# Kernel tuning notes

Hardware: AMD Instinct MI355X
Metric: run time of the kernel (lower is better)

## Reference

```python
import jax, jax.numpy as jnp
import numpy as np

WIN_SIZE = 11
SIGMA = 1.5
WEIGHTS = np.array([0.0448, 0.2856, 0.3001, 0.2363, 0.1333], dtype=np.float32)
K1, K2 = 0.01, 0.03
DATA_RANGE = 255.0
C1 = (K1 * DATA_RANGE) ** 2
C2 = (K2 * DATA_RANGE) ** 2
N_SCALES = 5


def _gauss1d():
    coords = np.arange(WIN_SIZE, dtype=np.float32) - WIN_SIZE // 2
    g = np.exp(-(coords ** 2) / (2.0 * SIGMA ** 2))
    g /= g.sum()
    return jnp.asarray(g, dtype=jnp.float32)


def _blur(x, g):
    # separable depthwise gaussian blur, VALID padding (matches pytorch_msssim)
    C = x.shape[1]
    wh = jnp.tile(g.reshape(1, 1, 1, WIN_SIZE), (C, 1, 1, 1))
    wv = jnp.tile(g.reshape(1, 1, WIN_SIZE, 1), (C, 1, 1, 1))
    dn = ('NCHW', 'OIHW', 'NCHW')
    x = jax.lax.conv_general_dilated(x, wh, (1, 1), 'VALID', dimension_numbers=dn, feature_group_count=C)
    x = jax.lax.conv_general_dilated(x, wv, (1, 1), 'VALID', dimension_numbers=dn, feature_group_count=C)
    return x


def _ssim(X, Y, g):
    mu1 = _blur(X, g)
    mu2 = _blur(Y, g)
    mu1_sq = mu1 * mu1
    mu2_sq = mu2 * mu2
    mu1_mu2 = mu1 * mu2
    sigma1_sq = _blur(X * X, g) - mu1_sq
    sigma2_sq = _blur(Y * Y, g) - mu2_sq
    sigma12 = _blur(X * Y, g) - mu1_mu2
    cs_map = (2.0 * sigma12 + C2) / (sigma1_sq + sigma2_sq + C2)
    ssim_map = ((2.0 * mu1_mu2 + C1) / (mu1_sq + mu2_sq + C1)) * cs_map
    return ssim_map.mean(axis=(2, 3)), cs_map.mean(axis=(2, 3))  # [B,C] each


def _avg_pool2(x):
    # avg_pool2d kernel=2 stride=2; H,W chosen even at every scale so padding=0
    return jax.lax.reduce_window(x, 0.0, jax.lax.add, (1, 1, 2, 2), (1, 1, 2, 2), 'VALID') / 4.0


def setup_inputs() -> dict:
    key = jax.random.key(0)
    k1, k2 = jax.random.split(key)
    shape = (32, 3, 384, 384)
    prediction = jax.random.uniform(k1, shape, dtype=jnp.float32) * DATA_RANGE
    truth = jax.random.uniform(k2, shape, dtype=jnp.float32) * DATA_RANGE
    return {"prediction": prediction, "truth": truth}


def reference(prediction, truth):
    g = _gauss1d()
    w = jnp.asarray(WEIGHTS)
    X, Y = prediction, truth
    mcs = []
    for i in range(N_SCALES):
        ssim_pc, cs = _ssim(X, Y, g)
        if i < N_SCALES - 1:
            mcs.append(jax.nn.relu(cs))
            X = _avg_pool2(X)
            Y = _avg_pool2(Y)
    vals = jnp.stack(mcs + [jax.nn.relu(ssim_pc)], axis=0)  # [5,B,C]
    ms_ssim_val = jnp.prod(vals ** w.reshape(-1, 1, 1), axis=0)  # [B,C]
    return 1.0 - ms_ssim_val.mean()
```

## Files before the change

### kernel.cpp

```cpp
#include <hip/hip_runtime.h>
#include <math.h>


namespace {

constexpr int NIMG = 96;
constexpr float TWO_C1 = 13.005f;
constexpr float TWO_C2 = 117.045f;

__device__ constexpr float GW[11] = {
    0.00102838f, 0.00759875f, 0.03600077f, 0.10936070f, 0.21300553f,
    0.26601172f,
    0.21300553f, 0.10936070f, 0.03600077f, 0.00759875f, 0.00102838f};

typedef float f2 __attribute__((ext_vector_type(2)));

__device__ __forceinline__ f2 pk(f2 a, f2 b, f2 c) {
#if __has_builtin(__builtin_elementwise_fma)
  return __builtin_elementwise_fma(a, b, c);
#else
  return a * b + c;
#endif
}

__device__ __forceinline__ float wshl1(float v) {
  return __int_as_float(__builtin_amdgcn_mov_dpp(
      __float_as_int(v), 0x130, 0xF, 0xF, true));
}

__device__ __forceinline__ f2 wshl1v(f2 v) {
  f2 r;
  r.x = wshl1(v.x);
  r.y = wshl1(v.y);
  return r;
}

struct SPtrs {
  const float* x[5];
  const float* y[5];
};

__global__ __launch_bounds__(256) void ssim_all(SPtrs sp,
                                                float* __restrict__ acc) {
  __shared__ float red[2][4];

  const int tile = blockIdx.x;
  int s;
  if (tile < 84) s = 0;
  else if (tile < 108) s = 1;
  else if (tile < 114) s = 2;
  else if (tile < 116) s = 3;
  else s = 4;
  const int tstart[5] = {0, 84, 108, 114, 116};
  const int HH[5] = {384, 192, 96, 48, 24};
  const int TXc[5] = {7, 4, 2, 1, 1};
  const int lt = tile - tstart[s];
  const int H = HH[s], W = H, OH = H - 10, OW = W - 10;
  const int tx = lt % TXc[s], ty = lt / TXc[s];
  const int img = blockIdx.z;
  const float* Xi = sp.x[s] + (size_t)img * H * W;
  const float* Yi = sp.y[s] + (size_t)img * H * W;
  const bool base = (s == 0);

  const int t = threadIdx.x;
  const int lane = t & 63, wv = t >> 6;
  const int col = tx * 54 + lane;
  const int cin = col < W - 1 ? col : W - 1;
  const int row0 = ty * 32 + wv * 8;

  f2 A[8] = {}, B[8] = {};
#pragma unroll
  for (int j = 0; j < 18; ++j) {
    int rin = row0 + j;
    rin = rin < H - 1 ? rin : H - 1;
    float a = Xi[(size_t)rin * W + cin];
    float b = Yi[(size_t)rin * W + cin];
    f2 P;
    P.x = base ? a + b : a;
    P.y = base ? a - b : b;
    f2 Q = P * P;
#pragma unroll
    for (int i = 0; i < 8; ++i) {
      const int k = j - i;
      if (k >= 0 && k <= 10) {
        const f2 wt = GW[k];
        A[i] = pk(wt, P, A[i]);
        B[i] = pk(wt, Q, B[i]);
      }
    }
  }

  const bool colok = (lane < 54) && (col < OW);
  float ssim_s = 0.f, cs_s = 0.f;
#pragma unroll
  for (int i = 0; i < 8; ++i) {
    f2 tA = A[i], tB = B[i];
    f2 bA = ((f2)GW[0]) * tA;
    f2 bB = ((f2)GW[0]) * tB;
#pragma unroll
    for (int k = 1; k <= 10; ++k) {
      const f2 wt = GW[k];
      tA = wshl1v(tA); bA = pk(wt, tA, bA);
      tB = wshl1v(tB); bB = pk(wt, tB, bB);
    }
    if (colok && (row0 + i < OH)) {
      float m2u = bA.x * bA.x, m2w = bA.y * bA.y;
      float Pm = m2u - m2w;
      float Qm = m2u + m2w;
      float Am = bB.x - bB.y;
      float Bm = bB.x + bB.y;
      float cs = (Am - Pm + TWO_C2) *
                 __builtin_amdgcn_rcpf(Bm - Qm + TWO_C2);
      float l = (Pm + TWO_C1) * __builtin_amdgcn_rcpf(Qm + TWO_C1);
      cs_s += cs;
      ssim_s += l * cs;
    }
  }

#pragma unroll
  for (int off = 32; off > 0; off >>= 1) {
    ssim_s += __shfl_down(ssim_s, off);
    cs_s += __shfl_down(cs_s, off);
  }
  if (lane == 0) { red[0][wv] = ssim_s; red[1][wv] = cs_s; }
  __syncthreads();
  if (t == 0) {
    atomicAdd(&acc[(2 * s + 0) * NIMG + img],
              red[0][0] + red[0][1] + red[0][2] + red[0][3]);
    atomicAdd(&acc[(2 * s + 1) * NIMG + img],
              red[1][0] + red[1][1] + red[1][2] + red[1][3]);
  }
}

__global__ __launch_bounds__(256) void pyramid_kernel(
    const float* __restrict__ X, const float* __restrict__ Y,
    float* __restrict__ u1, float* __restrict__ w1,
    float* __restrict__ u2, float* __restrict__ w2,
    float* __restrict__ u3, float* __restrict__ w3,
    float* __restrict__ u4, float* __restrict__ w4,
    float* __restrict__ acc) {
  const int img = blockIdx.y;
  const int t = threadIdx.x;
  if (blockIdx.x == 0 && img == 0) {
    for (int i = t; i < 10 * NIMG; i += 256) acc[i] = 0.f;
  }
  const int wv = t >> 6, lane = t & 63;
  const int tidx = blockIdx.x * 4 + wv;
  const int tx = tidx % 24, ty = tidx / 24;
  const int r = lane >> 3, c = lane & 7;

  const float* Xs = X + (size_t)img * 384 * 384;
  const float* Ys = Y + (size_t)img * 384 * 384;
  float* o1[2] = {u1 + (size_t)img * 192 * 192, w1 + (size_t)img * 192 * 192};
  float* o2[2] = {u2 + (size_t)img * 96 * 96,   w2 + (size_t)img * 96 * 96};
  float* o3[2] = {u3 + (size_t)img * 48 * 48,   w3 + (size_t)img * 48 * 48};
  float* o4[2] = {u4 + (size_t)img * 24 * 24,   w4 + (size_t)img * 24 * 24};

  int gr = ty * 16 + 2 * r, gc = tx * 16 + 2 * c;
  float2 xu = *(const float2*)&Xs[(size_t)gr * 384 + gc];
  float2 xv = *(const float2*)&Xs[(size_t)(gr + 1) * 384 + gc];
  float2 yu = *(const float2*)&Ys[(size_t)gr * 384 + gc];
  float2 yv = *(const float2*)&Ys[(size_t)(gr + 1) * 384 + gc];
  float l1x = 0.25f * (xu.x + xu.y + xv.x + xv.y);
  float l1y = 0.25f * (yu.x + yu.y + yv.x + yv.y);
  float ch0 = l1x + l1y, ch1 = l1x - l1y;
  float lv[2] = {ch0, ch1};

#pragma unroll
  for (int ch = 0; ch < 2; ++ch) {
    float l1 = lv[ch];
    o1[ch][(size_t)(ty * 8 + r) * 192 + tx * 8 + c] = l1;

    float l2 = l1 + __shfl_xor(l1, 1);
    l2 = 0.25f * (l2 + __shfl_xor(l2, 8));
    if ((r & 1) == 0 && (c & 1) == 0)
      o2[ch][(size_t)(ty * 4 + (r >> 1)) * 96 + tx * 4 + (c >> 1)] = l2;

    float l3 = l2 + __shfl_xor(l2, 2);
    l3 = 0.25f * (l3 + __shfl_xor(l3, 16));
    if ((r & 3) == 0 && (c & 3) == 0)
      o3[ch][(size_t)(ty * 2 + (r >> 2)) * 48 + tx * 2 + (c >> 2)] = l3;

    float l4 = l3 + __shfl_xor(l3, 4);
    l4 = 0.25f * (l4 + __shfl_xor(l4, 32));
    if (lane == 0) o4[ch][(size_t)ty * 24 + tx] = l4;
  }
}

__global__ void final_kernel(const float* __restrict__ acc,
                             float* __restrict__ out) {
  __shared__ float prods[NIMG];
  const float wts[5] = {0.0448f, 0.2856f, 0.3001f, 0.2363f, 0.1333f};
  const float inv_npix[5] = {1.f / (374.f * 374.f), 1.f / (182.f * 182.f),
                             1.f / (86.f * 86.f),  1.f / (38.f * 38.f),
                             1.f / (14.f * 14.f)};
  int t = threadIdx.x;
  if (t < NIMG) {
    float p = 1.f;
#pragma unroll
    for (int s = 0; s < 5; ++s) {
      float sum = (s < 4) ? acc[(s * 2 + 1) * NIMG + t]
                          : acc[(s * 2 + 0) * NIMG + t];
      float m = sum * inv_npix[s];
      m = m > 0.f ? m : 0.f;
      p *= powf(m, wts[s]);
    }
    prods[t] = p;
  }
  __syncthreads();
  if (t == 0) {
    float s = 0.f;
    for (int i = 0; i < NIMG; ++i) s += prods[i];
    out[0] = 1.f - s / (float)NIMG;
  }
}

}

extern "C" void kernel_launch(void* const* d_in, const int* in_sizes, int n_in,
                              void* d_out, int out_size, void* d_ws,
                              size_t ws_size, hipStream_t stream) {
  const float* X0 = (const float*)d_in[0];
  const float* Y0 = (const float*)d_in[1];
  float* out = (float*)d_out;
  float* ws = (float*)d_ws;

  const size_t L1 = (size_t)NIMG * 192 * 192;
  const size_t L2 = (size_t)NIMG * 96 * 96;
  const size_t L3 = (size_t)NIMG * 48 * 48;
  const size_t L4 = (size_t)NIMG * 24 * 24;

  float* u1 = ws;
  float* u2 = u1 + L1;
  float* u3 = u2 + L2;
  float* u4 = u3 + L3;
  float* w1 = u4 + L4;
  float* w2 = w1 + L1;
  float* w3 = w2 + L2;
  float* w4 = w3 + L3;
  float* acc = w4 + L4;

  pyramid_kernel<<<dim3(144, NIMG), dim3(256), 0, stream>>>(
      X0, Y0, u1, w1, u2, w2, u3, w3, u4, w4, acc);

  SPtrs sp;
  sp.x[0] = X0; sp.x[1] = u1; sp.x[2] = u2; sp.x[3] = u3; sp.x[4] = u4;
  sp.y[0] = Y0; sp.y[1] = w1; sp.y[2] = w2; sp.y[3] = w3; sp.y[4] = w4;

  ssim_all<<<dim3(117, 1, NIMG), dim3(256), 0, stream>>>(sp, acc);

  final_kernel<<<dim3(1), dim3(128), 0, stream>>>(acc, out);
}
```

Measured before the change: 238.9 us.

## Double rows per wave in SSIM kernel, add inline packed FMA and clamp-free paths

Each wave now computes 16 output rows instead of 8 from 26 input rows, so the 10-row vertical halo is amortised over more outputs and there are half as many tiles per image. Packed FMA and multiply are emitted through inline asm with splatted weight vectors. Templated variants drop the row clamp when the tile lies fully inside the image and skip the base/non-base select. The cost is higher register pressure from 32 f2 accumulators and fewer blocks to fill the GPU.

Measured after the change: 238.9 us. About the same (-0.0%).

```diff
diff --git a/kernel.cpp b/kernel.cpp
--- a/kernel.cpp
+++ b/kernel.cpp
@@ -15,19 +15,19 @@
 
 typedef float f2 __attribute__((ext_vector_type(2)));
 
-__device__ __forceinline__ f2 pk(f2 a, f2 b, f2 c) {
-#if __has_builtin(__builtin_elementwise_fma)
-  return __builtin_elementwise_fma(a, b, c);
-#else
-  return a * b + c;
-#endif
+__device__ __forceinline__ void pk_fma(f2& d, f2 a, f2 b) {
+  asm("v_pk_fma_f32 %0, %1, %2, %0" : "+v"(d) : "v"(a), "v"(b));
+}
+__device__ __forceinline__ f2 pk_mul(f2 a, f2 b) {
+  f2 d;
+  asm("v_pk_mul_f32 %0, %1, %2" : "=v"(d) : "v"(a), "v"(b));
+  return d;
 }
 
 __device__ __forceinline__ float wshl1(float v) {
   return __int_as_float(__builtin_amdgcn_mov_dpp(
       __float_as_int(v), 0x130, 0xF, 0xF, true));
 }
-
 __device__ __forceinline__ f2 wshl1v(f2 v) {
   f2 r;
   r.x = wshl1(v.x);
@@ -40,18 +40,50 @@
   const float* y[5];
 };
 
+template <bool BASE>
+__device__ __forceinline__ void tap(int j, float a, float b, f2 (&A)[16],
+                                    f2 (&B)[16], const f2 (&wtv)[11]) {
+  f2 P;
+  if (BASE) { P.x = a + b; P.y = a - b; }
+  else      { P.x = a;     P.y = b;     }
+  f2 Q = pk_mul(P, P);
+#pragma unroll
+  for (int i = 0; i < 16; ++i) {
+    const int k = j - i;
+    if (k >= 0 && k <= 10) {
+      pk_fma(A[i], wtv[k], P);
+      pk_fma(B[i], wtv[k], Q);
+    }
+  }
+}
+
+template <bool BASE, bool CLAMP>
+__device__ __forceinline__ void vblur(const float* __restrict__ Xi,
+                                      const float* __restrict__ Yi, int row0,
+                                      int W, int H, int cin, f2 (&A)[16],
+                                      f2 (&B)[16], const f2 (&wtv)[11]) {
+#pragma unroll
+  for (int j = 0; j < 26; ++j) {
+    int rin = row0 + j;
+    if (CLAMP) rin = rin < H - 1 ? rin : H - 1;
+    float a = Xi[(size_t)rin * W + cin];
+    float b = Yi[(size_t)rin * W + cin];
+    tap<BASE>(j, a, b, A, B, wtv);
+  }
+}
+
 __global__ __launch_bounds__(256) void ssim_all(SPtrs sp,
                                                 float* __restrict__ acc) {
   __shared__ float red[2][4];
 
   const int tile = blockIdx.x;
   int s;
-  if (tile < 84) s = 0;
-  else if (tile < 108) s = 1;
-  else if (tile < 114) s = 2;
-  else if (tile < 116) s = 3;
+  if (tile < 42) s = 0;
+  else if (tile < 54) s = 1;
+  else if (tile < 58) s = 2;
+  else if (tile < 59) s = 3;
   else s = 4;
-  const int tstart[5] = {0, 84, 108, 114, 116};
+  const int tstart[5] = {0, 42, 54, 58, 59};
   const int HH[5] = {384, 192, 96, 48, 24};
   const int TXc[5] = {7, 4, 2, 1, 1};
   const int lt = tile - tstart[s];
@@ -66,54 +98,48 @@
   const int lane = t & 63, wv = t >> 6;
   const int col = tx * 54 + lane;
   const int cin = col < W - 1 ? col : W - 1;
-  const int row0 = ty * 32 + wv * 8;
-
-  f2 A[8] = {}, B[8] = {};
-#pragma unroll
-  for (int j = 0; j < 18; ++j) {
-    int rin = row0 + j;
-    rin = rin < H - 1 ? rin : H - 1;
-    float a = Xi[(size_t)rin * W + cin];
-    float b = Yi[(size_t)rin * W + cin];
-    f2 P;
-    P.x = base ? a + b : a;
-    P.y = base ? a - b : b;
-    f2 Q = P * P;
-#pragma unroll
-    for (int i = 0; i < 8; ++i) {
-      const int k = j - i;
-      if (k >= 0 && k <= 10) {
-        const f2 wt = GW[k];
-        A[i] = pk(wt, P, A[i]);
-        B[i] = pk(wt, Q, B[i]);
+  const int row0 = ty * 64 + wv * 16;
+
+  f2 wtv[11];
+#pragma unroll
+  for (int k = 0; k < 11; ++k) { wtv[k].x = GW[k]; wtv[k].y = GW[k]; }
+
+  float ssim_s = 0.f, cs_s = 0.f;
+
+  if (row0 < OH) {
+    f2 A[16] = {}, B[16] = {};
+    const bool noclamp = (row0 + 25 <= H - 1);
+    if (base) {
+      if (noclamp) vblur<true, false>(Xi, Yi, row0, W, H, cin, A, B, wtv);
+      else         vblur<true, true >(Xi, Yi, row0, W, H, cin, A, B, wtv);
+    } else {
+      if (noclamp) vblur<false, false>(Xi, Yi, row0, W, H, cin, A, B, wtv);
+      else         vblur<false, true >(Xi, Yi, row0, W, H, cin, A, B, wtv);
+    }
+
+    const bool colok = (lane < 54) && (col < OW);
+#pragma unroll
+    for (int i = 0; i < 16; ++i) {
+      f2 tA = A[i], tB = B[i];
+      f2 bA = pk_mul(wtv[0], tA);
+      f2 bB = pk_mul(wtv[0], tB);
+#pragma unroll
+      for (int k = 1; k <= 10; ++k) {
+        tA = wshl1v(tA); pk_fma(bA, wtv[k], tA);
+        tB = wshl1v(tB); pk_fma(bB, wtv[k], tB);
       }
-    }
-  }
-
-  const bool colok = (lane < 54) && (col < OW);
-  float ssim_s = 0.f, cs_s = 0.f;
-#pragma unroll
-  for (int i = 0; i < 8; ++i) {
-    f2 tA = A[i], tB = B[i];
-    f2 bA = ((f2)GW[0]) * tA;
-    f2 bB = ((f2)GW[0]) * tB;
-#pragma unroll
-    for (int k = 1; k <= 10; ++k) {
-      const f2 wt = GW[k];
-      tA = wshl1v(tA); bA = pk(wt, tA, bA);
-      tB = wshl1v(tB); bB = pk(wt, tB, bB);
-    }
-    if (colok && (row0 + i < OH)) {
-      float m2u = bA.x * bA.x, m2w = bA.y * bA.y;
-      float Pm = m2u - m2w;
-      float Qm = m2u + m2w;
-      float Am = bB.x - bB.y;
-      float Bm = bB.x + bB.y;
-      float cs = (Am - Pm + TWO_C2) *
-                 __builtin_amdgcn_rcpf(Bm - Qm + TWO_C2);
-      float l = (Pm + TWO_C1) * __builtin_amdgcn_rcpf(Qm + TWO_C1);
-      cs_s += cs;
-      ssim_s += l * cs;
+      if (colok && (row0 + i < OH)) {
+        float m2u = bA.x * bA.x, m2w = bA.y * bA.y;
+        float Pm = m2u - m2w;
+        float Qm = m2u + m2w;
+        float Am = bB.x - bB.y;
+        float Bm = bB.x + bB.y;
+        float cs = (Am - Pm + TWO_C2) *
+                   __builtin_amdgcn_rcpf(Bm - Qm + TWO_C2);
+        float l = (Pm + TWO_C1) * __builtin_amdgcn_rcpf(Qm + TWO_C1);
+        cs_s += cs;
+        ssim_s += l * cs;
+      }
     }
   }
 
@@ -163,8 +189,7 @@
   float2 yv = *(const float2*)&Ys[(size_t)(gr + 1) * 384 + gc];
   float l1x = 0.25f * (xu.x + xu.y + xv.x + xv.y);
   float l1y = 0.25f * (yu.x + yu.y + yv.x + yv.y);
-  float ch0 = l1x + l1y, ch1 = l1x - l1y;
-  float lv[2] = {ch0, ch1};
+  float lv[2] = {l1x + l1y, l1x - l1y};
 
 #pragma unroll
   for (int ch = 0; ch < 2; ++ch) {
@@ -247,7 +272,7 @@
   sp.x[0] = X0; sp.x[1] = u1; sp.x[2] = u2; sp.x[3] = u3; sp.x[4] = u4;
   sp.y[0] = Y0; sp.y[1] = w1; sp.y[2] = w2; sp.y[3] = w3; sp.y[4] = w4;
 
-  ssim_all<<<dim3(117, 1, NIMG), dim3(256), 0, stream>>>(sp, acc);
+  ssim_all<<<dim3(60, 1, NIMG), dim3(256), 0, stream>>>(sp, acc);
 
   final_kernel<<<dim3(1), dim3(128), 0, stream>>>(acc, out);
 }
```
